# Optimization experiments

Hardware: AMD Instinct MI355X
Metric: run time of the kernel (lower is better)

Reference implementation:

```python
import jax, jax.numpy as jnp
import numpy as np

H, B, T, C = 1024, 256, 256, 10

def setup_inputs() -> dict:
    key = jax.random.key(0)
    ks = jax.random.split(key, 10)
    def xav(k, shape):
        fan_in, fan_out = shape[1], shape[0]
        lim = jnp.sqrt(6.0 / (fan_in + fan_out))
        return jax.random.uniform(k, shape, jnp.float32, -lim, lim)
    return {
        "x": jax.random.normal(ks[0], (B, T), jnp.float32),
        "W_gx": xav(ks[1], (H, 1)), "W_gh": xav(ks[2], (H, H)),
        "W_ix": xav(ks[3], (H, 1)), "W_ih": xav(ks[4], (H, H)),
        "W_fx": xav(ks[5], (H, 1)), "W_fh": xav(ks[6], (H, H)),
        "W_ox": xav(ks[7], (H, 1)), "W_oh": xav(ks[8], (H, H)),
        "W_ph": xav(ks[9], (C, H)),
        "b_g": jnp.zeros((B,), jnp.float32), "b_i": jnp.zeros((B,), jnp.float32),
        "b_f": jnp.zeros((B,), jnp.float32), "b_o": jnp.zeros((B,), jnp.float32),
        "b_p": jnp.zeros((B,), jnp.float32),
    }

def reference(x, W_gx, W_gh, W_ix, W_ih, W_fx, W_fh, W_ox, W_oh, W_ph,
              b_g, b_i, b_f, b_o, b_p):
    batch = x.shape[0]
    hidden = W_gh.shape[0]
    xs = x.T  # [T, B]; per-step x_t is a [1, B] row (input_dim = 1)

    def step(carry, x_t):
        h, c = carry                       # [H, B] each
        xr = x_t[None, :]                  # [1, B]
        g = jnp.tanh(W_gx @ xr + W_gh @ h + b_g)          # [H, B] + [B] broadcasts per column
        i = jax.nn.sigmoid(W_ix @ xr + W_ih @ h + b_i)
        f = jax.nn.sigmoid(W_fx @ xr + W_fh @ h + b_f)
        o = jax.nn.sigmoid(W_ox @ xr + W_oh @ h + b_o)
        c_new = g * i + c * f
        h_new = jnp.tanh(c_new) * o
        return (h_new, c_new), None

    h0 = jnp.zeros((hidden, batch), x.dtype)
    c0 = jnp.zeros((hidden, batch), x.dtype)
    (h_T, _), _ = jax.lax.scan(step, (h0, c0), xs)
    p = W_ph @ h_T + b_p                   # [C, B]
    y = jax.nn.softmax(p, axis=1)          # faithful: softmax over dim=1 (batch axis)
    return y.T                             # [B, C]
```

## Files before the change

kernel.cpp:

```cpp
#include <hip/hip_runtime.h>
#include <hip/hip_bf16.h>


#define H 1024
#define B 256
#define T 256
#define NCLS 10

typedef __attribute__((ext_vector_type(8))) short short8;
typedef __attribute__((ext_vector_type(4))) float f32x4;
typedef __attribute__((ext_vector_type(16))) float f32x16;
typedef unsigned long long ull;

__device__ inline unsigned short bf16_bits(float f) {
    union { __hip_bfloat16 h; unsigned short u; } cv;
    cv.h = __float2bfloat16(f);
    return cv.u;
}

#define L2E 1.4426950408889634f
__device__ inline float sigm_fast(float x) {
    float e = __builtin_amdgcn_exp2f(-L2E * x);
    return __builtin_amdgcn_rcpf(1.0f + e);
}
__device__ inline float tanh_fast(float x) {
    float e = __builtin_amdgcn_exp2f((2.0f * L2E) * x);
    return 1.0f - 2.0f * __builtin_amdgcn_rcpf(1.0f + e);
}


__global__ __launch_bounds__(512)
__attribute__((amdgpu_waves_per_eu(2, 2)))
void lstm_persist(
    const float* __restrict__ x,
    const float* __restrict__ Wgh, const float* __restrict__ Wih,
    const float* __restrict__ Wfh, const float* __restrict__ Woh,
    const float* __restrict__ Wgx, const float* __restrict__ Wix,
    const float* __restrict__ Wfx, const float* __restrict__ Wox,
    const float* __restrict__ bg, const float* __restrict__ bi,
    const float* __restrict__ bf_, const float* __restrict__ bo,
    char* __restrict__ frag,
    unsigned* __restrict__ flags,
    unsigned* __restrict__ det,
    float* __restrict__ hfin)
{
    __shared__ __align__(16) char hstage[65536];
    __shared__ __align__(16) float zb[16][32][32];
    __shared__ float wxl[4][32];
    __shared__ float bsl[4][32];
    __shared__ int sh_lcl;

    const int tid  = threadIdx.x;
    const int lane = tid & 63;
    const int wave = tid >> 6;
    const int gp   = wave >> 2;
    const int kq   = wave & 3;
    const int bt = blockIdx.x & 7;
    const int jt = blockIdx.x >> 3;
    const int j0 = jt * 32;
    const int b0 = bt * 32;

    unsigned xcc;
    __asm__ volatile("s_getreg_b32 %0, hwreg(HW_REG_XCC_ID)" : "=s"(xcc));
    xcc &= 7u;
    if (tid == 0)
        __hip_atomic_store(&det[bt * 32 + jt], xcc + 1u,
                           __ATOMIC_RELAXED, __HIP_MEMORY_SCOPE_AGENT);

    if (tid < 128) {
        int g = tid >> 5, r = tid & 31;
        const float* wx = (g == 0) ? Wgx : (g == 1) ? Wix : (g == 2) ? Wfx : Wox;
        const float* bb = (g == 0) ? bg  : (g == 1) ? bi  : (g == 2) ? bf_ : bo;
        wxl[g][r] = wx[j0 + r];
        bsl[g][r] = bb[b0 + r];
    }

    const float* Wlo = (gp == 0) ? Wgh : Wfh;
    const float* Whi = (gp == 0) ? Wih : Woh;
    short8 awreg[2][16];
#pragma unroll
    for (int gg = 0; gg < 2; ++gg) {
        const float* Wp = gg ? Whi : Wlo;
        const float* wrow = Wp + (j0 + (lane & 31)) * H
                          + kq * 256 + ((lane >> 5) * 8);
#pragma unroll
        for (int c = 0; c < 16; ++c) {
            const float4 f0 = *(const float4*)(wrow + c * 16);
            const float4 f1 = *(const float4*)(wrow + c * 16 + 4);
            short8 s;
            s[0] = (short)bf16_bits(f0.x); s[1] = (short)bf16_bits(f0.y);
            s[2] = (short)bf16_bits(f0.z); s[3] = (short)bf16_bits(f0.w);
            s[4] = (short)bf16_bits(f1.x); s[5] = (short)bf16_bits(f1.y);
            s[6] = (short)bf16_bits(f1.z); s[7] = (short)bf16_bits(f1.w);
            awreg[gg][c] = s;
        }
    }
#pragma unroll
    for (int gg = 0; gg < 2; ++gg)
#pragma unroll
        for (int c = 0; c < 16; ++c)
            __asm__ volatile("" : "+a"(awreg[gg][c]));

    if (wave == 0) {
        unsigned v;
        while (true) {
            v = __hip_atomic_load(&det[bt * 32 + (lane & 31)],
                                  __ATOMIC_RELAXED, __HIP_MEMORY_SCOPE_AGENT);
            if (__all((int)(v != 0u))) break;
            __builtin_amdgcn_s_sleep(1);
        }
        int same = __all((int)(v == xcc + 1u));
        if (tid == 0) sh_lcl = same;
    }
    __syncthreads();
    const bool lcl = (sh_lcl != 0);

    float creg[4] = {0.f, 0.f, 0.f, 0.f};
    const int nn = tid & 31;
    const int aa = tid >> 5;

    unsigned* myflag = &flags[blockIdx.x * 32];
    unsigned* pollflag = &flags[(((unsigned)lane & 31) * 8 + bt) * 32];

    for (int t = 0; t < T; ++t) {
        const float xv = x[(b0 + nn) * T + t];

        if (wave == 0) {
            const unsigned target = (unsigned)t;
            while (true) {
                unsigned v = __hip_atomic_load(pollflag, __ATOMIC_RELAXED,
                                               __HIP_MEMORY_SCOPE_AGENT);
                if (__all((int)(v >= target))) break;
                __builtin_amdgcn_s_sleep(1);
            }
        }
        __syncthreads();

        f32x16 acc0 = {0.f,0.f,0.f,0.f,0.f,0.f,0.f,0.f,
                       0.f,0.f,0.f,0.f,0.f,0.f,0.f,0.f};
        f32x16 acc1 = acc0;

        if (t > 0) {
            {
                const char* gbase = frag + (t & 1) * 524288 + bt * 65536 + tid * 16;
                short8 v0, v1, v2, v3, v4, v5, v6, v7;
                if (lcl) {
                    __asm__ volatile(
                        "global_load_dwordx4 %0, %8, off sc0\n\t"
                        "global_load_dwordx4 %1, %9, off sc0\n\t"
                        "global_load_dwordx4 %2, %10, off sc0\n\t"
                        "global_load_dwordx4 %3, %11, off sc0\n\t"
                        "global_load_dwordx4 %4, %12, off sc0\n\t"
                        "global_load_dwordx4 %5, %13, off sc0\n\t"
                        "global_load_dwordx4 %6, %14, off sc0\n\t"
                        "global_load_dwordx4 %7, %15, off sc0\n\t"
                        "s_waitcnt vmcnt(0)"
                        : "=&v"(v0), "=&v"(v1), "=&v"(v2), "=&v"(v3),
                          "=&v"(v4), "=&v"(v5), "=&v"(v6), "=&v"(v7)
                        : "v"(gbase),         "v"(gbase + 8192),
                          "v"(gbase + 16384), "v"(gbase + 24576),
                          "v"(gbase + 32768), "v"(gbase + 40960),
                          "v"(gbase + 49152), "v"(gbase + 57344)
                        : "memory");
                } else {
                    __asm__ volatile(
                        "global_load_dwordx4 %0, %8, off sc0 sc1\n\t"
                        "global_load_dwordx4 %1, %9, off sc0 sc1\n\t"
                        "global_load_dwordx4 %2, %10, off sc0 sc1\n\t"
                        "global_load_dwordx4 %3, %11, off sc0 sc1\n\t"
                        "global_load_dwordx4 %4, %12, off sc0 sc1\n\t"
                        "global_load_dwordx4 %5, %13, off sc0 sc1\n\t"
                        "global_load_dwordx4 %6, %14, off sc0 sc1\n\t"
                        "global_load_dwordx4 %7, %15, off sc0 sc1\n\t"
                        "s_waitcnt vmcnt(0)"
                        : "=&v"(v0), "=&v"(v1), "=&v"(v2), "=&v"(v3),
                          "=&v"(v4), "=&v"(v5), "=&v"(v6), "=&v"(v7)
                        : "v"(gbase),         "v"(gbase + 8192),
                          "v"(gbase + 16384), "v"(gbase + 24576),
                          "v"(gbase + 32768), "v"(gbase + 40960),
                          "v"(gbase + 49152), "v"(gbase + 57344)
                        : "memory");
                }
                short8* dd = (short8*)hstage;
                dd[tid +    0] = v0;  dd[tid +  512] = v1;
                dd[tid + 1024] = v2;  dd[tid + 1536] = v3;
                dd[tid + 2048] = v4;  dd[tid + 2560] = v5;
                dd[tid + 3072] = v6;  dd[tid + 3584] = v7;
            }
            __syncthreads();

#pragma unroll
            for (int c = 0; c < 16; ++c) {
                const int ks = (kq << 4) + c;
                short8 bf = *(const short8*)(hstage + ks * 1024 + lane * 16);
                acc0 = __builtin_amdgcn_mfma_f32_32x32x16_bf16(awreg[0][c], bf, acc0, 0, 0, 0);
                acc1 = __builtin_amdgcn_mfma_f32_32x32x16_bf16(awreg[1][c], bf, acc1, 0, 0, 0);
            }
        }

        {
            float* zbF = &zb[0][0][0];
            const int col = lane & 31;
            const int hi  = lane >> 5;
            const int g0 = gp * 2, g1 = g0 + 1;
#pragma unroll
            for (int rq = 0; rq < 4; ++rq) {
                const int sw = ((2 * rq + hi) ^ (col & 7)) << 2;
                f32x4 w0, w1;
#pragma unroll
                for (int e = 0; e < 4; ++e) {
                    w0[e] = acc0[rq * 4 + e];
                    w1[e] = acc1[rq * 4 + e];
                }
                *(f32x4*)(zbF + ((kq * 4 + g0) << 10) + (col << 5) + sw) = w0;
                *(f32x4*)(zbF + ((kq * 4 + g1) << 10) + (col << 5) + sw) = w1;
            }
        }
        __syncthreads();

        if (tid < 256) {
            const int r0 = aa * 4;
            const float* zbF = &zb[0][0][0];
            const int sw = (aa ^ (nn & 7)) << 2;
            f32x4 zs[4];
#pragma unroll
            for (int gi = 0; gi < 4; ++gi) {
                f32x4 s = *(const f32x4*)(zbF + (gi << 10) + (nn << 5) + sw);
#pragma unroll
                for (int kk = 1; kk < 4; ++kk)
                    s += *(const f32x4*)(zbF + (((kk << 2) + gi) << 10) + (nn << 5) + sw);
                zs[gi] = s;
            }
            unsigned short hb[4];
#pragma unroll
            for (int q = 0; q < 4; ++q) {
                const int row = r0 + q;
                float zg = zs[0][q] + wxl[0][row] * xv + bsl[0][nn];
                float zi = zs[1][q] + wxl[1][row] * xv + bsl[1][nn];
                float zf = zs[2][q] + wxl[2][row] * xv + bsl[2][nn];
                float zo = zs[3][q] + wxl[3][row] * xv + bsl[3][nn];
                float g  = tanh_fast(zg);
                float ig = sigm_fast(zi);
                float fg = sigm_fast(zf);
                float og = sigm_fast(zo);
                creg[q] = g * ig + creg[q] * fg;
                float hn = tanh_fast(creg[q]) * og;
                hb[q] = bf16_bits(hn);
                if (t == T - 1) hfin[(j0 + row) * B + (b0 + nn)] = hn;
            }
            const ull val = (ull)hb[0] | ((ull)hb[1] << 16)
                          | ((ull)hb[2] << 32) | ((ull)hb[3] << 48);
            const int jp = j0 + r0;
            short* fb = (short*)(frag + ((t + 1) & 1) * 524288) + bt * 32768;
            short* fdst = fb + (jp >> 4) * 512 + ((jp >> 3) & 1) * 256
                        + nn * 8 + (jp & 7);
            if (lcl) {
                *(volatile ull*)fdst = val;
            } else {
                __hip_atomic_store((ull*)fdst, val, __ATOMIC_RELAXED,
                                   __HIP_MEMORY_SCOPE_AGENT);
            }
        }

        __syncthreads();
        if (tid == 0) {
            __asm__ volatile("s_waitcnt vmcnt(0)" ::: "memory");
            __hip_atomic_store(myflag, (unsigned)(t + 1), __ATOMIC_RELAXED,
                               __HIP_MEMORY_SCOPE_AGENT);
        }
    }
}

__global__ __launch_bounds__(256) void lstm_final(
    const float* __restrict__ Wph, const float* __restrict__ hfin,
    const float* __restrict__ bp, float* __restrict__ out)
{
    __shared__ float sh[256];
    __shared__ float shm, shs;
    int c = blockIdx.x;
    int b = threadIdx.x;
    float acc = bp[b];
    const float* wr = Wph + c * H;
    for (int k = 0; k < H; ++k)
        acc += wr[k] * hfin[k * B + b];

    sh[b] = acc;
    __syncthreads();
    for (int s = 128; s > 0; s >>= 1) {
        if (b < s) sh[b] = fmaxf(sh[b], sh[b + s]);
        __syncthreads();
    }
    if (b == 0) shm = sh[0];
    __syncthreads();
    float e = expf(acc - shm);
    sh[b] = e;
    __syncthreads();
    for (int s = 128; s > 0; s >>= 1) {
        if (b < s) sh[b] += sh[b + s];
        __syncthreads();
    }
    if (b == 0) shs = sh[0];
    __syncthreads();
    out[b * NCLS + c] = e / shs;
}

extern "C" void kernel_launch(void* const* d_in, const int* in_sizes, int n_in,
                              void* d_out, int out_size, void* d_ws, size_t ws_size,
                              hipStream_t stream)
{
    const float* x   = (const float*)d_in[0];
    const float* Wgx = (const float*)d_in[1];
    const float* Wgh = (const float*)d_in[2];
    const float* Wix = (const float*)d_in[3];
    const float* Wih = (const float*)d_in[4];
    const float* Wfx = (const float*)d_in[5];
    const float* Wfh = (const float*)d_in[6];
    const float* Wox = (const float*)d_in[7];
    const float* Woh = (const float*)d_in[8];
    const float* Wph = (const float*)d_in[9];
    const float* bg  = (const float*)d_in[10];
    const float* bi  = (const float*)d_in[11];
    const float* bfv = (const float*)d_in[12];
    const float* bo  = (const float*)d_in[13];
    const float* bp  = (const float*)d_in[14];

    char* ws = (char*)d_ws;
    char* frag = ws;
    unsigned* flags = (unsigned*)(ws + 1048576);
    unsigned* det   = (unsigned*)(ws + 1081344);
    float* hfin = (float*)(ws + 1085440);

    hipMemsetAsync(flags, 0, 36864, stream);

    lstm_persist<<<256, 512, 0, stream>>>(
        x, Wgh, Wih, Wfh, Woh, Wgx, Wix, Wfx, Wox,
        bg, bi, bfv, bo, frag, flags, det, hfin);

    lstm_final<<<NCLS, 256, 0, stream>>>(Wph, hfin, bp, (float*)d_out);
}
```

Baseline: 1.211 ms.

## Stream h fragments directly into registers with per-wave polling and pipelined MFMA

Drops the LDS staging buffer for the previous hidden state. Each wave now polls only the flags of the producer blocks it needs, loads its own k-slice of h straight from global memory into registers, and interleaves staged waits with MFMAs so loads overlap compute. Two block-wide barriers per step go away. The gate nonlinearity stage is also spread over all 512 threads at 2 rows each instead of 256 threads at 4 rows, with narrower stores. This adds more polling traffic and more scattered 4-byte stores.

```diff
diff --git a/kernel.cpp b/kernel.cpp
--- a/kernel.cpp
+++ b/kernel.cpp
@@ -8,9 +8,9 @@
 #define NCLS 10
 
 typedef __attribute__((ext_vector_type(8))) short short8;
+typedef __attribute__((ext_vector_type(2))) float f32x2;
 typedef __attribute__((ext_vector_type(4))) float f32x4;
 typedef __attribute__((ext_vector_type(16))) float f32x16;
-typedef unsigned long long ull;
 
 __device__ inline unsigned short bf16_bits(float f) {
     union { __hip_bfloat16 h; unsigned short u; } cv;
@@ -28,6 +28,41 @@
     return 1.0f - 2.0f * __builtin_amdgcn_rcpf(1.0f + e);
 }
 
+
+#define LOADS4(d0, d1, d2, d3, PTR, SC)                                   \
+    __asm__ volatile(                                                     \
+        "global_load_dwordx4 %0, %4, off " SC "\n\t"                      \
+        "global_load_dwordx4 %1, %4, off offset:1024 " SC "\n\t"          \
+        "global_load_dwordx4 %2, %4, off offset:2048 " SC "\n\t"          \
+        "global_load_dwordx4 %3, %4, off offset:3072 " SC                  \
+        : "=&v"(d0), "=&v"(d1), "=&v"(d2), "=&v"(d3)                      \
+        : "v"(PTR));
+
+#define WAIT4(N, d0, d1, d2, d3)                                          \
+    __asm__ volatile("s_waitcnt vmcnt(" N ")"                             \
+        : "+v"(d0), "+v"(d1), "+v"(d2), "+v"(d3));
+
+#define MM(c, bb)                                                         \
+    acc0 = __builtin_amdgcn_mfma_f32_32x32x16_bf16(awreg[0][c], bb, acc0, 0, 0, 0); \
+    acc1 = __builtin_amdgcn_mfma_f32_32x32x16_bf16(awreg[1][c], bb, acc1, 0, 0, 0);
+
+#define GATE_MFMA(SC)                                                     \
+    {                                                                     \
+        short8 b0, b1, b2, b3, b4, b5, b6, b7;                            \
+        short8 b8, b9, b10, b11, b12, b13, b14, b15;                      \
+        LOADS4(b0, b1, b2, b3, gb, SC)                                    \
+        LOADS4(b4, b5, b6, b7, gb + 4096, SC)                             \
+        WAIT4("4", b0, b1, b2, b3)                                        \
+        MM(0, b0) MM(1, b1) MM(2, b2) MM(3, b3)                           \
+        LOADS4(b8, b9, b10, b11, gb + 8192, SC)                           \
+        LOADS4(b12, b13, b14, b15, gb + 12288, SC)                        \
+        WAIT4("8", b4, b5, b6, b7)                                        \
+        MM(4, b4) MM(5, b5) MM(6, b6) MM(7, b7)                           \
+        WAIT4("4", b8, b9, b10, b11)                                      \
+        MM(8, b8) MM(9, b9) MM(10, b10) MM(11, b11)                       \
+        WAIT4("0", b12, b13, b14, b15)                                    \
+        MM(12, b12) MM(13, b13) MM(14, b14) MM(15, b15)                   \
+    }
 
 __global__ __launch_bounds__(512)
 __attribute__((amdgpu_waves_per_eu(2, 2)))
@@ -44,7 +79,6 @@
     unsigned* __restrict__ det,
     float* __restrict__ hfin)
 {
-    __shared__ __align__(16) char hstage[65536];
     __shared__ __align__(16) float zb[16][32][32];
     __shared__ float wxl[4][32];
     __shared__ float bsl[4][32];
@@ -115,26 +149,15 @@
     __syncthreads();
     const bool lcl = (sh_lcl != 0);
 
-    float creg[4] = {0.f, 0.f, 0.f, 0.f};
+    float creg[2] = {0.f, 0.f};
     const int nn = tid & 31;
     const int aa = tid >> 5;
 
     unsigned* myflag = &flags[blockIdx.x * 32];
-    unsigned* pollflag = &flags[(((unsigned)lane & 31) * 8 + bt) * 32];
+    unsigned* pollflag = &flags[(((kq << 3) + (lane & 7)) * 8 + bt) * 32];
 
     for (int t = 0; t < T; ++t) {
         const float xv = x[(b0 + nn) * T + t];
-
-        if (wave == 0) {
-            const unsigned target = (unsigned)t;
-            while (true) {
-                unsigned v = __hip_atomic_load(pollflag, __ATOMIC_RELAXED,
-                                               __HIP_MEMORY_SCOPE_AGENT);
-                if (__all((int)(v >= target))) break;
-                __builtin_amdgcn_s_sleep(1);
-            }
-        }
-        __syncthreads();
 
         f32x16 acc0 = {0.f,0.f,0.f,0.f,0.f,0.f,0.f,0.f,
                        0.f,0.f,0.f,0.f,0.f,0.f,0.f,0.f};
@@ -142,59 +165,22 @@
 
         if (t > 0) {
             {
-                const char* gbase = frag + (t & 1) * 524288 + bt * 65536 + tid * 16;
-                short8 v0, v1, v2, v3, v4, v5, v6, v7;
-                if (lcl) {
-                    __asm__ volatile(
-                        "global_load_dwordx4 %0, %8, off sc0\n\t"
-                        "global_load_dwordx4 %1, %9, off sc0\n\t"
-                        "global_load_dwordx4 %2, %10, off sc0\n\t"
-                        "global_load_dwordx4 %3, %11, off sc0\n\t"
-                        "global_load_dwordx4 %4, %12, off sc0\n\t"
-                        "global_load_dwordx4 %5, %13, off sc0\n\t"
-                        "global_load_dwordx4 %6, %14, off sc0\n\t"
-                        "global_load_dwordx4 %7, %15, off sc0\n\t"
-                        "s_waitcnt vmcnt(0)"
-                        : "=&v"(v0), "=&v"(v1), "=&v"(v2), "=&v"(v3),
-                          "=&v"(v4), "=&v"(v5), "=&v"(v6), "=&v"(v7)
-                        : "v"(gbase),         "v"(gbase + 8192),
-                          "v"(gbase + 16384), "v"(gbase + 24576),
-                          "v"(gbase + 32768), "v"(gbase + 40960),
-                          "v"(gbase + 49152), "v"(gbase + 57344)
-                        : "memory");
-                } else {
-                    __asm__ volatile(
-                        "global_load_dwordx4 %0, %8, off sc0 sc1\n\t"
-                        "global_load_dwordx4 %1, %9, off sc0 sc1\n\t"
-                        "global_load_dwordx4 %2, %10, off sc0 sc1\n\t"
-                        "global_load_dwordx4 %3, %11, off sc0 sc1\n\t"
-                        "global_load_dwordx4 %4, %12, off sc0 sc1\n\t"
-                        "global_load_dwordx4 %5, %13, off sc0 sc1\n\t"
-                        "global_load_dwordx4 %6, %14, off sc0 sc1\n\t"
-                        "global_load_dwordx4 %7, %15, off sc0 sc1\n\t"
-                        "s_waitcnt vmcnt(0)"
-                        : "=&v"(v0), "=&v"(v1), "=&v"(v2), "=&v"(v3),
-                          "=&v"(v4), "=&v"(v5), "=&v"(v6), "=&v"(v7)
-                        : "v"(gbase),         "v"(gbase + 8192),
-                          "v"(gbase + 16384), "v"(gbase + 24576),
-                          "v"(gbase + 32768), "v"(gbase + 40960),
-                          "v"(gbase + 49152), "v"(gbase + 57344)
-                        : "memory");
+                const unsigned target = (unsigned)t;
+                while (true) {
+                    unsigned v = __hip_atomic_load(pollflag, __ATOMIC_RELAXED,
+                                                   __HIP_MEMORY_SCOPE_AGENT);
+                    if (__all((int)(v >= target))) break;
+                    __builtin_amdgcn_s_sleep(1);
                 }
-                short8* dd = (short8*)hstage;
-                dd[tid +    0] = v0;  dd[tid +  512] = v1;
-                dd[tid + 1024] = v2;  dd[tid + 1536] = v3;
-                dd[tid + 2048] = v4;  dd[tid + 2560] = v5;
-                dd[tid + 3072] = v6;  dd[tid + 3584] = v7;
-            }
-            __syncthreads();
-
-#pragma unroll
-            for (int c = 0; c < 16; ++c) {
-                const int ks = (kq << 4) + c;
-                short8 bf = *(const short8*)(hstage + ks * 1024 + lane * 16);
-                acc0 = __builtin_amdgcn_mfma_f32_32x32x16_bf16(awreg[0][c], bf, acc0, 0, 0, 0);
-                acc1 = __builtin_amdgcn_mfma_f32_32x32x16_bf16(awreg[1][c], bf, acc1, 0, 0, 0);
+            }
+            __asm__ volatile("" :: "v"(xv));
+
+            const char* gb = frag + (t & 1) * 524288 + bt * 65536
+                           + (kq << 14) + lane * 16;
+            if (lcl) {
+                GATE_MFMA("sc0")
+            } else {
+                GATE_MFMA("sc0 sc1")
             }
         }
 
@@ -218,27 +204,27 @@
         }
         __syncthreads();
 
-        if (tid < 256) {
-            const int r0 = aa * 4;
-            const float* zbF = &zb[0][0][0];
-            const int sw = (aa ^ (nn & 7)) << 2;
-            f32x4 zs[4];
+        {
+            const int grp = aa >> 1, half = aa & 1;
+            const float* zcol = &zb[0][0][0] + (nn << 5);
+            const int fo = ((grp ^ (nn & 7)) << 2) + (half << 1);
+            f32x2 zs[4];
 #pragma unroll
             for (int gi = 0; gi < 4; ++gi) {
-                f32x4 s = *(const f32x4*)(zbF + (gi << 10) + (nn << 5) + sw);
+                f32x2 s = *(const f32x2*)(zcol + (gi << 10) + fo);
 #pragma unroll
                 for (int kk = 1; kk < 4; ++kk)
-                    s += *(const f32x4*)(zbF + (((kk << 2) + gi) << 10) + (nn << 5) + sw);
+                    s += *(const f32x2*)(zcol + (((kk << 2) + gi) << 10) + fo);
                 zs[gi] = s;
             }
-            unsigned short hb[4];
-#pragma unroll
-            for (int q = 0; q < 4; ++q) {
-                const int row = r0 + q;
-                float zg = zs[0][q] + wxl[0][row] * xv + bsl[0][nn];
-                float zi = zs[1][q] + wxl[1][row] * xv + bsl[1][nn];
-                float zf = zs[2][q] + wxl[2][row] * xv + bsl[2][nn];
-                float zo = zs[3][q] + wxl[3][row] * xv + bsl[3][nn];
+            unsigned short hb[2];
+#pragma unroll
+            for (int q = 0; q < 2; ++q) {
+                const int jl = 2 * aa + q;
+                float zg = zs[0][q] + wxl[0][jl] * xv + bsl[0][nn];
+                float zi = zs[1][q] + wxl[1][jl] * xv + bsl[1][nn];
+                float zf = zs[2][q] + wxl[2][jl] * xv + bsl[2][nn];
+                float zo = zs[3][q] + wxl[3][jl] * xv + bsl[3][nn];
                 float g  = tanh_fast(zg);
                 float ig = sigm_fast(zi);
                 float fg = sigm_fast(zf);
@@ -246,18 +232,17 @@
                 creg[q] = g * ig + creg[q] * fg;
                 float hn = tanh_fast(creg[q]) * og;
                 hb[q] = bf16_bits(hn);
-                if (t == T - 1) hfin[(j0 + row) * B + (b0 + nn)] = hn;
-            }
-            const ull val = (ull)hb[0] | ((ull)hb[1] << 16)
-                          | ((ull)hb[2] << 32) | ((ull)hb[3] << 48);
-            const int jp = j0 + r0;
+                if (t == T - 1) hfin[(j0 + jl) * B + (b0 + nn)] = hn;
+            }
+            const unsigned val = (unsigned)hb[0] | ((unsigned)hb[1] << 16);
+            const int jj = j0 + 2 * aa;
             short* fb = (short*)(frag + ((t + 1) & 1) * 524288) + bt * 32768;
-            short* fdst = fb + (jp >> 4) * 512 + ((jp >> 3) & 1) * 256
-                        + nn * 8 + (jp & 7);
+            short* fdst = fb + (jj >> 4) * 512 + ((jj >> 3) & 1) * 256
+                        + nn * 8 + (jj & 7);
             if (lcl) {
-                *(volatile ull*)fdst = val;
+                *(volatile unsigned*)fdst = val;
             } else {
-                __hip_atomic_store((ull*)fdst, val, __ATOMIC_RELAXED,
+                __hip_atomic_store((unsigned*)fdst, val, __ATOMIC_RELAXED,
                                    __HIP_MEMORY_SCOPE_AGENT);
             }
         }
```

After: 1.190 ms. Within noise of the previous version (-1.7%).
